# Kernel tuning notes

Hardware: AMD Instinct MI355X
Metric: run time of the kernel (lower is better)

Reference implementation:

```python
import jax, jax.numpy as jnp
import numpy as np

H = 16            # num_heads
SEG = 2048        # segment_size
DIL = 8           # dilation_rate
BLOCK_M = 64      # triton query block size (min(64, M_padded))


def setup_inputs() -> dict:
    key = jax.random.key(0)
    k1, k2, k3 = jax.random.split(key, 3)
    B, M, D = 2, 8192, 1024
    x = jax.random.normal(k1, (B, M, D), dtype=jnp.float32)
    Wqkv = jax.random.normal(k2, (3 * D, D), dtype=jnp.float32) * 0.02
    Wout = jax.random.normal(k3, (D, D), dtype=jnp.float32) * 0.02
    return {"x": x, "Wqkv": Wqkv, "Wout": Wout}


def reference(x, Wqkv, Wout):
    B, M, D = x.shape
    hd = D // H
    scale = hd ** -0.5
    S = M // SEG                      # number of segments (M is a multiple of SEG)
    Kn = SEG // DIL                   # dilated keys per segment
    nb = SEG // BLOCK_M               # query blocks per segment

    # qkv projection (torch Linear: x @ W^T), split into q,k,v: [B,H,M,hd]
    qkv = jnp.einsum('bmd,ed->bme', x, Wqkv).reshape(B, M, 3, H, hd)
    qkv = jnp.transpose(qkv, (2, 0, 3, 1, 4))
    q, k, v = qkv[0] * scale, qkv[1], qkv[2]

    # segment-local views
    q4 = q.reshape(B, H, S, SEG, hd)
    k4 = k.reshape(B, H, S, SEG, hd)[:, :, :, ::DIL]   # [B,H,S,Kn,hd] dilated keys
    v4 = v.reshape(B, H, S, SEG, hd)[:, :, :, ::DIL]

    # scores per segment: [B,H,S,SEG,Kn]
    scores = jnp.einsum('bhspd,bhskd->bhspk', q4, k4)
    # kernel normalization: per key j, subtract max over the 64-query block
    scores = scores.reshape(B, H, S, nb, BLOCK_M, Kn)
    c = jnp.max(scores, axis=4, keepdims=True)          # [B,H,S,nb,1,Kn]
    w = jnp.exp(scores - c)
    den = jnp.sum(w, axis=-1) + 1e-10                   # [B,H,S,nb,BLOCK_M]
    num = jnp.einsum('bhsnmk,bhskd->bhsnmd', w, v4)
    out = num / den[..., None]                          # [B,H,S,nb,BLOCK_M,hd]

    out = out.reshape(B, H, M, hd)
    out = jnp.transpose(out, (0, 2, 1, 3)).reshape(B, M, D)
    return jnp.einsum('bmd,ed->bme', out, Wout)
```

## Files before the change

### kernel.cpp

```cpp
#include <hip/hip_runtime.h>
#include <hip/hip_bf16.h>
#include <stdint.h>


typedef __attribute__((ext_vector_type(8))) short short8;
typedef __attribute__((ext_vector_type(4))) float f32x4;

#define DEVI static __device__ __forceinline__

DEVI unsigned short f2bf(float f) {
  union { float f; uint32_t u; } v; v.f = f;
  return (unsigned short)((v.u + 0x7FFFu + ((v.u >> 16) & 1u)) >> 16);
}

DEVI uint32_t pack_bf16(float lo, float hi) {
  return (uint32_t)f2bf(lo) | ((uint32_t)f2bf(hi) << 16);
}

DEVI uint32_t pack_hu(float lo, float hi) {
  union { float f; uint32_t u; } a, b; a.f = lo; b.f = hi;
  return ((a.u + 0x8000u) >> 16) | ((b.u + 0x8000u) & 0xFFFF0000u);
}

DEVI void gload_lds16(const void* g, void* l) {
  __builtin_amdgcn_global_load_lds((const __attribute__((address_space(1))) void*)g,
                                   (__attribute__((address_space(3))) void*)l,
                                   16, 0, 0);
}

__global__ void cvt_all(const float* __restrict__ x, const float* __restrict__ wqkv,
                        const float* __restrict__ wout,
                        unsigned short* __restrict__ xb, unsigned short* __restrict__ wqkvb,
                        unsigned short* __restrict__ woutb) {
  long i = ((long)blockIdx.x * 256 + threadIdx.x) * 4;
  const float* src; unsigned short* dst; long off;
  if (i < 16777216)          { src = x;    dst = xb;    off = i; }
  else if (i < 19922944)     { src = wqkv; dst = wqkvb; off = i - 16777216; }
  else                       { src = wout; dst = woutb; off = i - 19922944; }
  float4 f = *(const float4*)(src + off);
  uint2 o;
  o.x = (uint32_t)f2bf(f.x) | ((uint32_t)f2bf(f.y) << 16);
  o.y = (uint32_t)f2bf(f.z) | ((uint32_t)f2bf(f.w) << 16);
  *(uint2*)(dst + off) = o;
}

#define STAGE_A(bf, hf, kt) do { \
  gload_lds16(Abase + (long)((hf) * 128 + srow0) * 1024 + (kt) * 64 + scol0, &smA[bf][hf][se0]); \
  gload_lds16(Abase + (long)((hf) * 128 + srow1) * 1024 + (kt) * 64 + scol1, &smA[bf][hf][se1]); \
} while (0)
#define STAGE_B(bf, hf, kt) do { \
  gload_lds16(Bbase + (long)((hf) * 128 + srow0) * 1024 + (kt) * 64 + scol0, &smB[bf][hf][se0]); \
  gload_lds16(Bbase + (long)((hf) * 128 + srow1) * 1024 + (kt) * 64 + scol1, &smB[bf][hf][se1]); \
} while (0)

template<bool OUT_F32>
__global__ __launch_bounds__(512, 1) void gemm8p(
    const unsigned short* __restrict__ A, const unsigned short* __restrict__ B,
    void* __restrict__ Cv, float scale)
{
  __shared__ unsigned short smA[2][2][128 * 64];
  __shared__ unsigned short smB[2][2][128 * 64];
  const int tid = threadIdx.x;
  const int tm = blockIdx.x, tn = blockIdx.y;
  const int w = tid >> 6, lane = tid & 63;
  const int wm = w >> 2, wn = w & 3;
  const int lr = lane & 15, lq = lane >> 4;

  const int e0 = tid * 8,        e1 = (512 + tid) * 8;
  const int srow0 = e0 >> 6,     srow1 = e1 >> 6;
  const int sc0 = (e0 >> 3) & 7, sc1 = (e1 >> 3) & 7;
  const int scol0 = (sc0 ^ (srow0 & 7)) * 8, scol1 = (sc1 ^ (srow1 & 7)) * 8;
  const int se0 = e0, se1 = e1;

  const unsigned short* Abase = A + (long)tm * 256 * 1024;
  const unsigned short* Bbase = B + (long)tn * 256 * 1024;

  f32x4 acc[8][4] = {};
  short8 af[4][2];
  short8 bfr[2][2][2];

  STAGE_A(0, 0, 0); STAGE_B(0, 0, 0); STAGE_B(0, 1, 0); STAGE_A(0, 1, 0);
  asm volatile("s_waitcnt vmcnt(4)" ::: "memory");
  __builtin_amdgcn_s_barrier();
  asm volatile("" ::: "memory");

  for (int t = 0; t < 8; ++t) {
#pragma unroll
    for (int p = 0; p < 8; ++p) {
      const int o = p >> 2;
      const int q = p & 3;
      const int a = (p >> 1) & 1;
      const int b = a ^ (q & 1);

      if (q == 0 || q == 2) {
#pragma unroll
        for (int mi2 = 0; mi2 < 4; ++mi2) {
          int r = wm * 64 + mi2 * 16 + lr;
#pragma unroll
          for (int kk = 0; kk < 2; ++kk) {
            int kc = kk * 4 + lq;
            af[mi2][kk] = *(const short8*)&smA[o][a][r * 64 + ((kc ^ (r & 7)) * 8)];
          }
        }
      }
      if (q == 0 || q == 1) {
#pragma unroll
        for (int nj2 = 0; nj2 < 2; ++nj2) {
          int r = wn * 32 + nj2 * 16 + lr;
#pragma unroll
          for (int kk = 0; kk < 2; ++kk) {
            int kc = kk * 4 + lq;
            bfr[b][nj2][kk] = *(const short8*)&smB[o][b][r * 64 + ((kc ^ (r & 7)) * 8)];
          }
        }
      }

      switch (p) {
        case 0: STAGE_A(1, 0, 2 * t + 1); STAGE_B(1, 0, 2 * t + 1); break;
        case 2: STAGE_B(1, 1, 2 * t + 1); STAGE_A(1, 1, 2 * t + 1); break;
        case 4: if (t < 7) { STAGE_A(0, 0, 2 * t + 2); STAGE_B(0, 0, 2 * t + 2); } break;
        case 6: if (t < 7) { STAGE_B(0, 1, 2 * t + 2); STAGE_A(0, 1, 2 * t + 2); } break;
      }

      __builtin_amdgcn_s_barrier();
      asm volatile("" ::: "memory");

      __builtin_amdgcn_s_setprio(1);
#pragma unroll
      for (int kk = 0; kk < 2; ++kk)
#pragma unroll
        for (int mi2 = 0; mi2 < 4; ++mi2)
#pragma unroll
          for (int nj2 = 0; nj2 < 2; ++nj2)
            acc[a * 4 + mi2][b * 2 + nj2] = __builtin_amdgcn_mfma_f32_16x16x32_bf16(
                af[mi2][kk], bfr[b][nj2][kk], acc[a * 4 + mi2][b * 2 + nj2], 0, 0, 0);
      __builtin_amdgcn_s_setprio(0);

      if (t < 7) {
        if (p == 0 || p == 3 || p == 4 || p == 7)
          asm volatile("s_waitcnt vmcnt(4)" ::: "memory");
      } else {
        if (p == 0 || p == 3)  asm volatile("s_waitcnt vmcnt(4)" ::: "memory");
        else if (p == 4)       asm volatile("s_waitcnt vmcnt(0)" ::: "memory");
      }
      __builtin_amdgcn_s_barrier();
      asm volatile("" ::: "memory");
    }
  }

  if (OUT_F32) {
    float* scratch = (float*)&smA[0][0][0] + w * 544;
    float* Cf = (float*)Cv;
#pragma unroll
    for (int ai = 0; ai < 8; ++ai) {
#pragma unroll
      for (int b2 = 0; b2 < 2; ++b2) {
#pragma unroll
        for (int nj2 = 0; nj2 < 2; ++nj2)
#pragma unroll
          for (int rr = 0; rr < 4; ++rr)
            scratch[(lq * 4 + rr) * 33 + nj2 * 16 + lr] = acc[ai][b2 * 2 + nj2][rr] * scale;
        asm volatile("s_waitcnt lgkmcnt(0)" ::: "memory");
        __builtin_amdgcn_sched_barrier(0);
        int rr2 = lane >> 2, cb = (lane & 3) * 8;
        float4 v0, v1;
        v0.x = scratch[rr2 * 33 + cb + 0]; v0.y = scratch[rr2 * 33 + cb + 1];
        v0.z = scratch[rr2 * 33 + cb + 2]; v0.w = scratch[rr2 * 33 + cb + 3];
        v1.x = scratch[rr2 * 33 + cb + 4]; v1.y = scratch[rr2 * 33 + cb + 5];
        v1.z = scratch[rr2 * 33 + cb + 6]; v1.w = scratch[rr2 * 33 + cb + 7];
        asm volatile("s_waitcnt lgkmcnt(0)" ::: "memory");
        __builtin_amdgcn_sched_barrier(0);
        long rowg = tm * 256 + wm * 64 + (ai & 3) * 16 + (ai >> 2) * 128 + rr2;
        long colg = tn * 256 + wn * 32 + b2 * 128 + cb;
        *(float4*)&Cf[rowg * 1024 + colg] = v0;
        *(float4*)&Cf[rowg * 1024 + colg + 4] = v1;
      }
    }
  } else {
    const int row0 = tm * 256 + wm * 64 + lq * 4;
    const int col0 = tn * 256 + wn * 32 + lr;
#pragma unroll
    for (int mi = 0; mi < 8; ++mi) {
      int row = row0 + (mi & 3) * 16 + (mi >> 2) * 128;
#pragma unroll
      for (int nj = 0; nj < 4; ++nj) {
        int col = col0 + (nj & 1) * 16 + (nj >> 1) * 128;
#pragma unroll
        for (int rr = 0; rr < 4; ++rr)
          ((unsigned short*)Cv)[(long)(row + rr) * 1024 + col] = f2bf(acc[mi][nj][rr] * scale);
      }
    }
  }
}

template<int EPI>
__global__ __launch_bounds__(256, 2) void gemm_bt(
    const unsigned short* __restrict__ A, const unsigned short* __restrict__ B,
    void* __restrict__ Cv, unsigned short* __restrict__ Cv2,
    float scale, long a_row_stride, int ldc, int K)
{
  __shared__ unsigned short smA[128 * 64];
  __shared__ unsigned short smB[128 * 64];
  const int tid = threadIdx.x;
  const int tm = blockIdx.x, tn = blockIdx.y;
  const int w = tid >> 6, lane = tid & 63;
  const int wr = (w >> 1) * 64, wc = (w & 1) * 64;
  const int lr = lane & 15, lq = lane >> 4;

  int se[4], srow[4], scol[4];
#pragma unroll
  for (int i = 0; i < 4; ++i) {
    int e = (i * 256 + tid) * 8;
    int r = e >> 6;
    int cc = (e >> 3) & 7;
    se[i] = e; srow[i] = r; scol[i] = (cc ^ (r & 7)) * 8;
  }

  f32x4 acc[4][4] = {};

  for (int kt = 0; kt < K / 64; ++kt) {
    if (kt) __syncthreads();
#pragma unroll
    for (int i = 0; i < 4; ++i)
      gload_lds16(A + (long)(tm * 128 + srow[i]) * a_row_stride + kt * 64 + scol[i], &smA[se[i]]);
#pragma unroll
    for (int i = 0; i < 4; ++i)
      gload_lds16(B + (long)(tn * 128 + srow[i]) * K + kt * 64 + scol[i], &smB[se[i]]);
    __syncthreads();

#pragma unroll
    for (int kk = 0; kk < 2; ++kk) {
      int kc = kk * 4 + lq;
      short8 af[4], bfm[4];
#pragma unroll
      for (int i = 0; i < 4; ++i) {
        int row = wr + i * 16 + lr;
        af[i] = *(const short8*)&smA[row * 64 + ((kc ^ (row & 7)) * 8)];
      }
#pragma unroll
      for (int j = 0; j < 4; ++j) {
        int row = wc + j * 16 + lr;
        bfm[j] = *(const short8*)&smB[row * 64 + ((kc ^ (row & 7)) * 8)];
      }
#pragma unroll
      for (int i = 0; i < 4; ++i)
#pragma unroll
        for (int j = 0; j < 4; ++j)
          acc[i][j] = __builtin_amdgcn_mfma_f32_16x16x32_bf16(af[i], bfm[j], acc[i][j], 0, 0, 0);
    }
  }

  if (EPI == 2 && tn >= 8) {
    const int fbase = (tn - 8) * 128 + wc;
#pragma unroll
    for (int ip = 0; ip < 4; ip += 2) {
      int t0 = tm * 128 + wr + ip * 16 + lq * 4;
      int seg = t0 >> 8;
      int ts  = t0 & 255;
      int c32 = (ts >> 5) * 16 + (ts & 15);
#pragma unroll
      for (int j = 0; j < 4; ++j) {
        int f = fbase + j * 16 + lr;
        uint32_t* rp = (uint32_t*)&Cv2[((long)(seg * 1024 + f)) * 256];
        uint4 U;
        U.x = pack_bf16(acc[ip][j][0] * scale, acc[ip + 1][j][0] * scale);
        U.y = pack_bf16(acc[ip][j][1] * scale, acc[ip + 1][j][1] * scale);
        U.z = pack_bf16(acc[ip][j][2] * scale, acc[ip + 1][j][2] * scale);
        U.w = pack_bf16(acc[ip][j][3] * scale, acc[ip + 1][j][3] * scale);
        *(uint4*)&rp[c32] = U;
      }
    }
    return;
  }

#pragma unroll
  for (int i = 0; i < 4; ++i) {
    int rg0 = tm * 128 + wr + i * 16 + lq * 4;
#pragma unroll
    for (int j = 0; j < 4; ++j) {
      int cg = tn * 128 + wc + j * 16 + lr;
#pragma unroll
      for (int r = 0; r < 4; ++r) {
        float v = acc[i][j][r] * scale;
        long off = (long)(rg0 + r) * ldc + cg;
        if (EPI == 0) ((float*)Cv)[off] = v;
        else          ((unsigned short*)Cv)[off] = f2bf(v);
      }
    }
  }
}

__global__ __launch_bounds__(512, 2) void attn_kernel(
    const unsigned short* __restrict__ qb,
    const unsigned short* __restrict__ kb,
    const unsigned short* __restrict__ vtb,
    unsigned short* __restrict__ attout)
{
  __shared__ unsigned short v_t[64 * 256];
  __shared__ uint32_t w32[8][64][20];

  const int u = (blockIdx.x & 7) * 64 + (blockIdx.x >> 3);
  const int quarter = u & 3, h = (u >> 2) & 15, s = (u >> 6) & 3, b = u >> 8;
  const int tid = threadIdx.x, w = tid >> 6, lane = tid & 63;
  const int lr = lane & 15, lq = lane >> 4;
  const long qrow0 = (long)b * 8192 + s * 2048 + quarter * 512 + w * 64;
  const int hc = h * 64;

  const unsigned short* kbase = kb + ((long)(b * 4 + s) * 256) * 1024 + hc;
  const unsigned short* vbase = vtb + ((long)(b * 4 + s) * 1024 + hc) * 256;

#pragma unroll
  for (int it = 0; it < 4; ++it) {
    int e = (it * 512 + tid) * 8;
    int f = e >> 8;
    int ch = (e >> 3) & 31;
    gload_lds16(vbase + (long)f * 256 + ((ch ^ (f & 7)) * 8), &v_t[e]);
  }

  const unsigned short* qbase = qb + qrow0 * 1024 + hc;
  short8 aq[4][2];
#pragma unroll
  for (int i = 0; i < 4; ++i)
#pragma unroll
    for (int kk = 0; kk < 2; ++kk)
      aq[i][kk] = *(const short8*)&qbase[(i * 16 + lr) * 1024 + (kk * 4 + lq) * 8];

  __syncthreads();

  short8 ones;
#pragma unroll
  for (int e = 0; e < 8; ++e) ones[e] = (short)0x3F80;

  uint32_t (*wsl)[20] = w32[w];

  f32x4 acc_pv[4][4] = {};
  f32x4 acc_den[4] = {};
  short8 bk0[2][2], bk1[2][2];
  f32x4 sA[4][2], sB[4][2];

#define LOADK(BK, CC) do { \
  _Pragma("unroll") for (int j = 0; j < 2; ++j) \
    _Pragma("unroll") for (int kk = 0; kk < 2; ++kk) \
      BK[j][kk] = *(const short8*)&kbase[(long)((CC) * 32 + j * 16 + lr) * 1024 + (kk * 4 + lq) * 8]; \
} while (0)

#define QKT(S, BK) do { \
  _Pragma("unroll") for (int i = 0; i < 4; ++i) \
    _Pragma("unroll") for (int j = 0; j < 2; ++j) { \
      f32x4 z = {0.f, 0.f, 0.f, 0.f}; S[i][j] = z; } \
  _Pragma("unroll") for (int kk = 0; kk < 2; ++kk) \
    _Pragma("unroll") for (int i = 0; i < 4; ++i) \
      _Pragma("unroll") for (int j = 0; j < 2; ++j) \
        S[i][j] = __builtin_amdgcn_mfma_f32_16x16x32_bf16(aq[i][kk], BK[j][kk], S[i][j], 0, 0, 0); \
} while (0)

#define SOFTPV(S, CC) do { \
  short8 av_[4]; \
  _Pragma("unroll") for (int ct = 0; ct < 4; ++ct) { \
    int frow = ct * 16 + lr; \
    av_[ct] = *(const short8*)&v_t[frow * 256 + ((((CC) * 4 + lq) ^ (frow & 7)) << 3)]; } \
  float p0[4], p1[4]; \
  _Pragma("unroll") for (int i = 0; i < 4; ++i) { \
    p0[i] = fmaxf(fmaxf(S[i][0][0], S[i][0][1]), fmaxf(S[i][0][2], S[i][0][3])); \
    p1[i] = fmaxf(fmaxf(S[i][1][0], S[i][1][1]), fmaxf(S[i][1][2], S[i][1][3])); \
  } \
  float c0 = fmaxf(fmaxf(p0[0], p0[1]), fmaxf(p0[2], p0[3])); \
  float c1 = fmaxf(fmaxf(p1[0], p1[1]), fmaxf(p1[2], p1[3])); \
  c0 = fmaxf(c0, __shfl_xor(c0, 16)); c0 = fmaxf(c0, __shfl_xor(c0, 32)); \
  c1 = fmaxf(c1, __shfl_xor(c1, 16)); c1 = fmaxf(c1, __shfl_xor(c1, 32)); \
  _Pragma("unroll") for (int uu = 0; uu < 4; ++uu) { \
    _Pragma("unroll") for (int r = 0; r < 4; ++r) { \
      int qq = uu * 16 + lq * 4 + r; \
      wsl[qq][lr] = pack_hu(__expf(S[uu][0][r] - c0), __expf(S[uu][1][r] - c1)); } \
    short8 bw = *(const short8*)&wsl[uu * 16 + lr][lq * 4]; \
    acc_den[uu] = __builtin_amdgcn_mfma_f32_16x16x32_bf16(ones, bw, acc_den[uu], 0, 0, 0); \
    _Pragma("unroll") for (int ct = 0; ct < 4; ++ct) \
      acc_pv[uu][ct] = __builtin_amdgcn_mfma_f32_16x16x32_bf16(av_[ct], bw, acc_pv[uu][ct], 0, 0, 0); \
  } \
} while (0)

  LOADK(bk0, 0);
  LOADK(bk1, 1);
  QKT(sA, bk0);

  LOADK(bk0, 2); QKT(sB, bk1); SOFTPV(sA, 0);
  LOADK(bk1, 3); QKT(sA, bk0); SOFTPV(sB, 1);
  LOADK(bk0, 4); QKT(sB, bk1); SOFTPV(sA, 2);
  LOADK(bk1, 5); QKT(sA, bk0); SOFTPV(sB, 3);
  LOADK(bk0, 6); QKT(sB, bk1); SOFTPV(sA, 4);
  LOADK(bk1, 7); QKT(sA, bk0); SOFTPV(sB, 5);
                 QKT(sB, bk1); SOFTPV(sA, 6);
                               SOFTPV(sB, 7);

#pragma unroll
  for (int qi = 0; qi < 4; ++qi) {
    float inv = 1.0f / (acc_den[qi][0] + 1e-10f);
    long orow = (qrow0 + qi * 16 + lr) * 1024 + hc;
#pragma unroll
    for (int ct = 0; ct < 4; ++ct) {
      uint2 p;
      p.x = pack_hu(acc_pv[qi][ct][0] * inv, acc_pv[qi][ct][1] * inv);
      p.y = pack_hu(acc_pv[qi][ct][2] * inv, acc_pv[qi][ct][3] * inv);
      *(uint2*)&attout[orow + ct * 16 + lq * 4] = p;
    }
  }
}

extern "C" void kernel_launch(void* const* d_in, const int* in_sizes, int n_in,
                              void* d_out, int out_size, void* d_ws, size_t ws_size,
                              hipStream_t stream) {
  (void)in_sizes; (void)n_in; (void)out_size; (void)ws_size;
  const float* x    = (const float*)d_in[0];
  const float* Wqkv = (const float*)d_in[1];
  const float* Wout = (const float*)d_in[2];
  float* out = (float*)d_out;
  char* ws = (char*)d_ws;

  unsigned short* xb     = (unsigned short*)(ws);
  unsigned short* attout = (unsigned short*)(ws);
  unsigned short* wqkvb  = (unsigned short*)(ws + 33554432);
  unsigned short* woutb  = (unsigned short*)(ws + 39845888);
  unsigned short* qbuf   = (unsigned short*)(ws + 41943040);
  unsigned short* kbuf   = (unsigned short*)(ws + 75497472);
  unsigned short* vtb    = (unsigned short*)(ws + 79691776);

  cvt_all<<<20480, 256, 0, stream>>>(x, Wqkv, Wout, xb, wqkvb, woutb);

  gemm8p<false><<<dim3(64, 4), 512, 0, stream>>>(xb, wqkvb, (void*)qbuf, 0.125f);
  gemm_bt<2><<<dim3(16, 16), 256, 0, stream>>>(
      xb, wqkvb + 1024 * 1024, (void*)kbuf, vtb, 1.0f, 8192, 1024, 1024);

  attn_kernel<<<512, 512, 0, stream>>>(qbuf, kbuf, vtb, attout);

  gemm8p<true><<<dim3(64, 4), 512, 0, stream>>>(attout, woutb, (void*)out, 1.0f);
}
```

Measured before the change: 162.8 us.

## Merge Q and K/V projections into one launch; shrink attention blocks

The Q projection and the dilated K/V projection now run in a single 320-block launch. Blocks 0-255 compute Q with the 256x256 pipelined tile, and blocks 256-319 compute K and transposed V over only the dilated rows, reusing the same main loop (now shared through a macro). This removes one kernel launch and the weaker 128x128 gemm_bt path. The attention kernel is also split into 1024 blocks of 256 threads with occupancy hint 3, instead of 512 blocks of 512 threads, to improve load balance and occupancy. The trade-off is that the K/V blocks run a heavier tile serially alongside the Q blocks, and the attention kernel reloads the V tile twice as often.

```diff
diff --git a/kernel.cpp b/kernel.cpp
--- a/kernel.cpp
+++ b/kernel.cpp
@@ -44,24 +44,95 @@
   *(uint2*)(dst + off) = o;
 }
 
+#define GEMM8P_MAINLOOP(ASTRIDE)                                               \
+  f32x4 acc[8][4] = {};                                                        \
+  short8 af[4][2];                                                             \
+  short8 bfr[2][2][2];                                                         \
+  STAGE_A(0, 0, 0); STAGE_B(0, 0, 0); STAGE_B(0, 1, 0); STAGE_A(0, 1, 0);      \
+  asm volatile("s_waitcnt vmcnt(4)" ::: "memory");                             \
+  __builtin_amdgcn_s_barrier();                                                \
+  asm volatile("" ::: "memory");                                               \
+  for (int t = 0; t < 8; ++t) {                                                \
+    _Pragma("unroll")                                                          \
+    for (int p = 0; p < 8; ++p) {                                              \
+      const int o = p >> 2;                                                    \
+      const int q = p & 3;                                                     \
+      const int a = (p >> 1) & 1;                                              \
+      const int b = a ^ (q & 1);                                               \
+      if (q == 0 || q == 2) {                                                  \
+        _Pragma("unroll")                                                      \
+        for (int mi2 = 0; mi2 < 4; ++mi2) {                                    \
+          int r = wm * 64 + mi2 * 16 + lr;                                     \
+          _Pragma("unroll")                                                    \
+          for (int kk = 0; kk < 2; ++kk) {                                     \
+            int kc = kk * 4 + lq;                                              \
+            af[mi2][kk] = *(const short8*)&smA[o][a][r * 64 + ((kc ^ (r & 7)) * 8)]; \
+          }                                                                    \
+        }                                                                      \
+      }                                                                        \
+      if (q == 0 || q == 1) {                                                  \
+        _Pragma("unroll")                                                      \
+        for (int nj2 = 0; nj2 < 2; ++nj2) {                                    \
+          int r = wn * 32 + nj2 * 16 + lr;                                     \
+          _Pragma("unroll")                                                    \
+          for (int kk = 0; kk < 2; ++kk) {                                     \
+            int kc = kk * 4 + lq;                                              \
+            bfr[b][nj2][kk] = *(const short8*)&smB[o][b][r * 64 + ((kc ^ (r & 7)) * 8)]; \
+          }                                                                    \
+        }                                                                      \
+      }                                                                        \
+      switch (p) {                                                             \
+        case 0: STAGE_A(1, 0, 2 * t + 1); STAGE_B(1, 0, 2 * t + 1); break;     \
+        case 2: STAGE_B(1, 1, 2 * t + 1); STAGE_A(1, 1, 2 * t + 1); break;     \
+        case 4: if (t < 7) { STAGE_A(0, 0, 2 * t + 2); STAGE_B(0, 0, 2 * t + 2); } break; \
+        case 6: if (t < 7) { STAGE_B(0, 1, 2 * t + 2); STAGE_A(0, 1, 2 * t + 2); } break; \
+      }                                                                        \
+      __builtin_amdgcn_s_barrier();                                            \
+      asm volatile("" ::: "memory");                                           \
+      __builtin_amdgcn_s_setprio(1);                                           \
+      _Pragma("unroll")                                                        \
+      for (int kk = 0; kk < 2; ++kk)                                           \
+        _Pragma("unroll")                                                      \
+        for (int mi2 = 0; mi2 < 4; ++mi2)                                      \
+          _Pragma("unroll")                                                    \
+          for (int nj2 = 0; nj2 < 2; ++nj2)                                    \
+            acc[a * 4 + mi2][b * 2 + nj2] = __builtin_amdgcn_mfma_f32_16x16x32_bf16( \
+                af[mi2][kk], bfr[b][nj2][kk], acc[a * 4 + mi2][b * 2 + nj2], 0, 0, 0); \
+      __builtin_amdgcn_s_setprio(0);                                           \
+      if (t < 7) {                                                             \
+        if (p == 0 || p == 3 || p == 4 || p == 7)                              \
+          asm volatile("s_waitcnt vmcnt(4)" ::: "memory");                     \
+      } else {                                                                 \
+        if (p == 0 || p == 3)  asm volatile("s_waitcnt vmcnt(4)" ::: "memory"); \
+        else if (p == 4)       asm volatile("s_waitcnt vmcnt(0)" ::: "memory"); \
+      }                                                                        \
+      __builtin_amdgcn_s_barrier();                                            \
+      asm volatile("" ::: "memory");                                           \
+    }                                                                          \
+  }
+
 #define STAGE_A(bf, hf, kt) do { \
-  gload_lds16(Abase + (long)((hf) * 128 + srow0) * 1024 + (kt) * 64 + scol0, &smA[bf][hf][se0]); \
-  gload_lds16(Abase + (long)((hf) * 128 + srow1) * 1024 + (kt) * 64 + scol1, &smA[bf][hf][se1]); \
+  gload_lds16(Abase + (long)((hf) * 128 + srow0) * AST + (kt) * 64 + scol0, &smA[bf][hf][se0]); \
+  gload_lds16(Abase + (long)((hf) * 128 + srow1) * AST + (kt) * 64 + scol1, &smA[bf][hf][se1]); \
 } while (0)
 #define STAGE_B(bf, hf, kt) do { \
   gload_lds16(Bbase + (long)((hf) * 128 + srow0) * 1024 + (kt) * 64 + scol0, &smB[bf][hf][se0]); \
   gload_lds16(Bbase + (long)((hf) * 128 + srow1) * 1024 + (kt) * 64 + scol1, &smB[bf][hf][se1]); \
 } while (0)
 
-template<bool OUT_F32>
-__global__ __launch_bounds__(512, 1) void gemm8p(
-    const unsigned short* __restrict__ A, const unsigned short* __restrict__ B,
-    void* __restrict__ Cv, float scale)
+__global__ __launch_bounds__(512, 1) void gemm_qkv(
+    const unsigned short* __restrict__ xb, const unsigned short* __restrict__ wqkvb,
+    unsigned short* __restrict__ qbuf, unsigned short* __restrict__ kbuf,
+    unsigned short* __restrict__ vtb)
 {
   __shared__ unsigned short smA[2][2][128 * 64];
   __shared__ unsigned short smB[2][2][128 * 64];
+  const int bid = blockIdx.x;
+  const bool isQ = bid < 256;
+  const int tm = isQ ? (bid & 63) : ((bid - 256) & 7);
+  const int tn = isQ ? (bid >> 6) : ((bid - 256) >> 3);
+  const long AST = isQ ? 1024 : 8192;
   const int tid = threadIdx.x;
-  const int tm = blockIdx.x, tn = blockIdx.y;
   const int w = tid >> 6, lane = tid & 63;
   const int wm = w >> 2, wn = w & 3;
   const int lr = lane & 15, lq = lane >> 4;
@@ -72,111 +143,12 @@
   const int scol0 = (sc0 ^ (srow0 & 7)) * 8, scol1 = (sc1 ^ (srow1 & 7)) * 8;
   const int se0 = e0, se1 = e1;
 
-  const unsigned short* Abase = A + (long)tm * 256 * 1024;
-  const unsigned short* Bbase = B + (long)tn * 256 * 1024;
-
-  f32x4 acc[8][4] = {};
-  short8 af[4][2];
-  short8 bfr[2][2][2];
-
-  STAGE_A(0, 0, 0); STAGE_B(0, 0, 0); STAGE_B(0, 1, 0); STAGE_A(0, 1, 0);
-  asm volatile("s_waitcnt vmcnt(4)" ::: "memory");
-  __builtin_amdgcn_s_barrier();
-  asm volatile("" ::: "memory");
-
-  for (int t = 0; t < 8; ++t) {
-#pragma unroll
-    for (int p = 0; p < 8; ++p) {
-      const int o = p >> 2;
-      const int q = p & 3;
-      const int a = (p >> 1) & 1;
-      const int b = a ^ (q & 1);
-
-      if (q == 0 || q == 2) {
-#pragma unroll
-        for (int mi2 = 0; mi2 < 4; ++mi2) {
-          int r = wm * 64 + mi2 * 16 + lr;
-#pragma unroll
-          for (int kk = 0; kk < 2; ++kk) {
-            int kc = kk * 4 + lq;
-            af[mi2][kk] = *(const short8*)&smA[o][a][r * 64 + ((kc ^ (r & 7)) * 8)];
-          }
-        }
-      }
-      if (q == 0 || q == 1) {
-#pragma unroll
-        for (int nj2 = 0; nj2 < 2; ++nj2) {
-          int r = wn * 32 + nj2 * 16 + lr;
-#pragma unroll
-          for (int kk = 0; kk < 2; ++kk) {
-            int kc = kk * 4 + lq;
-            bfr[b][nj2][kk] = *(const short8*)&smB[o][b][r * 64 + ((kc ^ (r & 7)) * 8)];
-          }
-        }
-      }
-
-      switch (p) {
-        case 0: STAGE_A(1, 0, 2 * t + 1); STAGE_B(1, 0, 2 * t + 1); break;
-        case 2: STAGE_B(1, 1, 2 * t + 1); STAGE_A(1, 1, 2 * t + 1); break;
-        case 4: if (t < 7) { STAGE_A(0, 0, 2 * t + 2); STAGE_B(0, 0, 2 * t + 2); } break;
-        case 6: if (t < 7) { STAGE_B(0, 1, 2 * t + 2); STAGE_A(0, 1, 2 * t + 2); } break;
-      }
-
-      __builtin_amdgcn_s_barrier();
-      asm volatile("" ::: "memory");
-
-      __builtin_amdgcn_s_setprio(1);
-#pragma unroll
-      for (int kk = 0; kk < 2; ++kk)
-#pragma unroll
-        for (int mi2 = 0; mi2 < 4; ++mi2)
-#pragma unroll
-          for (int nj2 = 0; nj2 < 2; ++nj2)
-            acc[a * 4 + mi2][b * 2 + nj2] = __builtin_amdgcn_mfma_f32_16x16x32_bf16(
-                af[mi2][kk], bfr[b][nj2][kk], acc[a * 4 + mi2][b * 2 + nj2], 0, 0, 0);
-      __builtin_amdgcn_s_setprio(0);
-
-      if (t < 7) {
-        if (p == 0 || p == 3 || p == 4 || p == 7)
-          asm volatile("s_waitcnt vmcnt(4)" ::: "memory");
-      } else {
-        if (p == 0 || p == 3)  asm volatile("s_waitcnt vmcnt(4)" ::: "memory");
-        else if (p == 4)       asm volatile("s_waitcnt vmcnt(0)" ::: "memory");
-      }
-      __builtin_amdgcn_s_barrier();
-      asm volatile("" ::: "memory");
-    }
-  }
-
-  if (OUT_F32) {
-    float* scratch = (float*)&smA[0][0][0] + w * 544;
-    float* Cf = (float*)Cv;
-#pragma unroll
-    for (int ai = 0; ai < 8; ++ai) {
-#pragma unroll
-      for (int b2 = 0; b2 < 2; ++b2) {
-#pragma unroll
-        for (int nj2 = 0; nj2 < 2; ++nj2)
-#pragma unroll
-          for (int rr = 0; rr < 4; ++rr)
-            scratch[(lq * 4 + rr) * 33 + nj2 * 16 + lr] = acc[ai][b2 * 2 + nj2][rr] * scale;
-        asm volatile("s_waitcnt lgkmcnt(0)" ::: "memory");
-        __builtin_amdgcn_sched_barrier(0);
-        int rr2 = lane >> 2, cb = (lane & 3) * 8;
-        float4 v0, v1;
-        v0.x = scratch[rr2 * 33 + cb + 0]; v0.y = scratch[rr2 * 33 + cb + 1];
-        v0.z = scratch[rr2 * 33 + cb + 2]; v0.w = scratch[rr2 * 33 + cb + 3];
-        v1.x = scratch[rr2 * 33 + cb + 4]; v1.y = scratch[rr2 * 33 + cb + 5];
-        v1.z = scratch[rr2 * 33 + cb + 6]; v1.w = scratch[rr2 * 33 + cb + 7];
-        asm volatile("s_waitcnt lgkmcnt(0)" ::: "memory");
-        __builtin_amdgcn_sched_barrier(0);
-        long rowg = tm * 256 + wm * 64 + (ai & 3) * 16 + (ai >> 2) * 128 + rr2;
-        long colg = tn * 256 + wn * 32 + b2 * 128 + cb;
-        *(float4*)&Cf[rowg * 1024 + colg] = v0;
-        *(float4*)&Cf[rowg * 1024 + colg + 4] = v1;
-      }
-    }
-  } else {
+  const unsigned short* Abase = xb + (long)tm * 256 * AST;
+  const unsigned short* Bbase = (isQ ? wqkvb : wqkvb + 1024 * 1024) + (long)tn * 256 * 1024;
+
+  GEMM8P_MAINLOOP(AST)
+
+  if (isQ) {
     const int row0 = tm * 256 + wm * 64 + lq * 4;
     const int col0 = tn * 256 + wn * 32 + lr;
 #pragma unroll
@@ -187,131 +159,119 @@
         int col = col0 + (nj & 1) * 16 + (nj >> 1) * 128;
 #pragma unroll
         for (int rr = 0; rr < 4; ++rr)
-          ((unsigned short*)Cv)[(long)(row + rr) * 1024 + col] = f2bf(acc[mi][nj][rr] * scale);
+          qbuf[(long)(row + rr) * 1024 + col] = f2bf(acc[mi][nj][rr] * 0.125f);
       }
     }
-  }
-}
-
-template<int EPI>
-__global__ __launch_bounds__(256, 2) void gemm_bt(
-    const unsigned short* __restrict__ A, const unsigned short* __restrict__ B,
-    void* __restrict__ Cv, unsigned short* __restrict__ Cv2,
-    float scale, long a_row_stride, int ldc, int K)
-{
-  __shared__ unsigned short smA[128 * 64];
-  __shared__ unsigned short smB[128 * 64];
-  const int tid = threadIdx.x;
-  const int tm = blockIdx.x, tn = blockIdx.y;
-  const int w = tid >> 6, lane = tid & 63;
-  const int wr = (w >> 1) * 64, wc = (w & 1) * 64;
-  const int lr = lane & 15, lq = lane >> 4;
-
-  int se[4], srow[4], scol[4];
-#pragma unroll
-  for (int i = 0; i < 4; ++i) {
-    int e = (i * 256 + tid) * 8;
-    int r = e >> 6;
-    int cc = (e >> 3) & 7;
-    se[i] = e; srow[i] = r; scol[i] = (cc ^ (r & 7)) * 8;
-  }
-
-  f32x4 acc[4][4] = {};
-
-  for (int kt = 0; kt < K / 64; ++kt) {
-    if (kt) __syncthreads();
-#pragma unroll
-    for (int i = 0; i < 4; ++i)
-      gload_lds16(A + (long)(tm * 128 + srow[i]) * a_row_stride + kt * 64 + scol[i], &smA[se[i]]);
-#pragma unroll
-    for (int i = 0; i < 4; ++i)
-      gload_lds16(B + (long)(tn * 128 + srow[i]) * K + kt * 64 + scol[i], &smB[se[i]]);
-    __syncthreads();
-
-#pragma unroll
-    for (int kk = 0; kk < 2; ++kk) {
-      int kc = kk * 4 + lq;
-      short8 af[4], bfm[4];
-#pragma unroll
-      for (int i = 0; i < 4; ++i) {
-        int row = wr + i * 16 + lr;
-        af[i] = *(const short8*)&smA[row * 64 + ((kc ^ (row & 7)) * 8)];
+  } else if (tn < 4) {
+    const int row0 = tm * 256 + wm * 64 + lq * 4;
+    const int col0 = tn * 256 + wn * 32 + lr;
+#pragma unroll
+    for (int mi = 0; mi < 8; ++mi) {
+      int row = row0 + (mi & 3) * 16 + (mi >> 2) * 128;
+#pragma unroll
+      for (int nj = 0; nj < 4; ++nj) {
+        int col = col0 + (nj & 1) * 16 + (nj >> 1) * 128;
+#pragma unroll
+        for (int rr = 0; rr < 4; ++rr)
+          kbuf[(long)(row + rr) * 1024 + col] = f2bf(acc[mi][nj][rr]);
       }
-#pragma unroll
-      for (int j = 0; j < 4; ++j) {
-        int row = wc + j * 16 + lr;
-        bfm[j] = *(const short8*)&smB[row * 64 + ((kc ^ (row & 7)) * 8)];
-      }
-#pragma unroll
-      for (int i = 0; i < 4; ++i)
-#pragma unroll
-        for (int j = 0; j < 4; ++j)
-          acc[i][j] = __builtin_amdgcn_mfma_f32_16x16x32_bf16(af[i], bfm[j], acc[i][j], 0, 0, 0);
-    }
-  }
-
-  if (EPI == 2 && tn >= 8) {
-    const int fbase = (tn - 8) * 128 + wc;
-#pragma unroll
-    for (int ip = 0; ip < 4; ip += 2) {
-      int t0 = tm * 128 + wr + ip * 16 + lq * 4;
+    }
+  } else {
+#pragma unroll
+    for (int mi = 0; mi < 8; mi += 2) {
+      int t0 = tm * 256 + wm * 64 + (mi & 3) * 16 + (mi >> 2) * 128 + lq * 4;
       int seg = t0 >> 8;
       int ts  = t0 & 255;
       int c32 = (ts >> 5) * 16 + (ts & 15);
 #pragma unroll
-      for (int j = 0; j < 4; ++j) {
-        int f = fbase + j * 16 + lr;
-        uint32_t* rp = (uint32_t*)&Cv2[((long)(seg * 1024 + f)) * 256];
+      for (int nj = 0; nj < 4; ++nj) {
+        int f = (tn - 4) * 256 + wn * 32 + (nj & 1) * 16 + (nj >> 1) * 128 + lr;
+        uint32_t* rp = (uint32_t*)&vtb[((long)(seg * 1024 + f)) * 256];
         uint4 U;
-        U.x = pack_bf16(acc[ip][j][0] * scale, acc[ip + 1][j][0] * scale);
-        U.y = pack_bf16(acc[ip][j][1] * scale, acc[ip + 1][j][1] * scale);
-        U.z = pack_bf16(acc[ip][j][2] * scale, acc[ip + 1][j][2] * scale);
-        U.w = pack_bf16(acc[ip][j][3] * scale, acc[ip + 1][j][3] * scale);
+        U.x = pack_bf16(acc[mi][nj][0], acc[mi + 1][nj][0]);
+        U.y = pack_bf16(acc[mi][nj][1], acc[mi + 1][nj][1]);
+        U.z = pack_bf16(acc[mi][nj][2], acc[mi + 1][nj][2]);
+        U.w = pack_bf16(acc[mi][nj][3], acc[mi + 1][nj][3]);
         *(uint4*)&rp[c32] = U;
       }
     }
-    return;
-  }
-
-#pragma unroll
-  for (int i = 0; i < 4; ++i) {
-    int rg0 = tm * 128 + wr + i * 16 + lq * 4;
-#pragma unroll
-    for (int j = 0; j < 4; ++j) {
-      int cg = tn * 128 + wc + j * 16 + lr;
-#pragma unroll
-      for (int r = 0; r < 4; ++r) {
-        float v = acc[i][j][r] * scale;
-        long off = (long)(rg0 + r) * ldc + cg;
-        if (EPI == 0) ((float*)Cv)[off] = v;
-        else          ((unsigned short*)Cv)[off] = f2bf(v);
-      }
-    }
-  }
-}
-
-__global__ __launch_bounds__(512, 2) void attn_kernel(
+  }
+}
+
+__global__ __launch_bounds__(512, 1) void gemm_out(
+    const unsigned short* __restrict__ A, const unsigned short* __restrict__ B,
+    float* __restrict__ Cf)
+{
+  __shared__ unsigned short smA[2][2][128 * 64];
+  __shared__ unsigned short smB[2][2][128 * 64];
+  const int tm = blockIdx.x, tn = blockIdx.y;
+  const long AST = 1024;
+  const int tid = threadIdx.x;
+  const int w = tid >> 6, lane = tid & 63;
+  const int wm = w >> 2, wn = w & 3;
+  const int lr = lane & 15, lq = lane >> 4;
+
+  const int e0 = tid * 8,        e1 = (512 + tid) * 8;
+  const int srow0 = e0 >> 6,     srow1 = e1 >> 6;
+  const int sc0 = (e0 >> 3) & 7, sc1 = (e1 >> 3) & 7;
+  const int scol0 = (sc0 ^ (srow0 & 7)) * 8, scol1 = (sc1 ^ (srow1 & 7)) * 8;
+  const int se0 = e0, se1 = e1;
+
+  const unsigned short* Abase = A + (long)tm * 256 * 1024;
+  const unsigned short* Bbase = B + (long)tn * 256 * 1024;
+
+  GEMM8P_MAINLOOP(AST)
+
+  float* scratch = (float*)&smA[0][0][0] + w * 544;
+#pragma unroll
+  for (int ai = 0; ai < 8; ++ai) {
+#pragma unroll
+    for (int b2 = 0; b2 < 2; ++b2) {
+#pragma unroll
+      for (int nj2 = 0; nj2 < 2; ++nj2)
+#pragma unroll
+        for (int rr = 0; rr < 4; ++rr)
+          scratch[(lq * 4 + rr) * 33 + nj2 * 16 + lr] = acc[ai][b2 * 2 + nj2][rr];
+      asm volatile("s_waitcnt lgkmcnt(0)" ::: "memory");
+      __builtin_amdgcn_sched_barrier(0);
+      int rr2 = lane >> 2, cb = (lane & 3) * 8;
+      float4 v0, v1;
+      v0.x = scratch[rr2 * 33 + cb + 0]; v0.y = scratch[rr2 * 33 + cb + 1];
+      v0.z = scratch[rr2 * 33 + cb + 2]; v0.w = scratch[rr2 * 33 + cb + 3];
+      v1.x = scratch[rr2 * 33 + cb + 4]; v1.y = scratch[rr2 * 33 + cb + 5];
+      v1.z = scratch[rr2 * 33 + cb + 6]; v1.w = scratch[rr2 * 33 + cb + 7];
+      asm volatile("s_waitcnt lgkmcnt(0)" ::: "memory");
+      __builtin_amdgcn_sched_barrier(0);
+      long rowg = tm * 256 + wm * 64 + (ai & 3) * 16 + (ai >> 2) * 128 + rr2;
+      long colg = tn * 256 + wn * 32 + b2 * 128 + cb;
+      *(float4*)&Cf[rowg * 1024 + colg] = v0;
+      *(float4*)&Cf[rowg * 1024 + colg + 4] = v1;
+    }
+  }
+}
+
+__global__ __launch_bounds__(256, 3) void attn_kernel(
     const unsigned short* __restrict__ qb,
     const unsigned short* __restrict__ kb,
     const unsigned short* __restrict__ vtb,
     unsigned short* __restrict__ attout)
 {
   __shared__ unsigned short v_t[64 * 256];
-  __shared__ uint32_t w32[8][64][20];
-
-  const int u = (blockIdx.x & 7) * 64 + (blockIdx.x >> 3);
-  const int quarter = u & 3, h = (u >> 2) & 15, s = (u >> 6) & 3, b = u >> 8;
+  __shared__ uint32_t w32[4][64][20];
+
+  const int u = (blockIdx.x & 7) * 128 + (blockIdx.x >> 3);
+  const int e8 = u & 7, h = (u >> 3) & 15, s = (u >> 7) & 3, b = u >> 9;
   const int tid = threadIdx.x, w = tid >> 6, lane = tid & 63;
   const int lr = lane & 15, lq = lane >> 4;
-  const long qrow0 = (long)b * 8192 + s * 2048 + quarter * 512 + w * 64;
+  const long qrow0 = (long)b * 8192 + s * 2048 + e8 * 256 + w * 64;
   const int hc = h * 64;
 
   const unsigned short* kbase = kb + ((long)(b * 4 + s) * 256) * 1024 + hc;
   const unsigned short* vbase = vtb + ((long)(b * 4 + s) * 1024 + hc) * 256;
 
 #pragma unroll
-  for (int it = 0; it < 4; ++it) {
-    int e = (it * 512 + tid) * 8;
+  for (int it = 0; it < 8; ++it) {
+    int e = (it * 256 + tid) * 8;
     int f = e >> 8;
     int ch = (e >> 3) & 31;
     gload_lds16(vbase + (long)f * 256 + ((ch ^ (f & 7)) * 8), &v_t[e]);
@@ -426,11 +386,9 @@
 
   cvt_all<<<20480, 256, 0, stream>>>(x, Wqkv, Wout, xb, wqkvb, woutb);
 
-  gemm8p<false><<<dim3(64, 4), 512, 0, stream>>>(xb, wqkvb, (void*)qbuf, 0.125f);
-  gemm_bt<2><<<dim3(16, 16), 256, 0, stream>>>(
-      xb, wqkvb + 1024 * 1024, (void*)kbuf, vtb, 1.0f, 8192, 1024, 1024);
-
-  attn_kernel<<<512, 512, 0, stream>>>(qbuf, kbuf, vtb, attout);
-
-  gemm8p<true><<<dim3(64, 4), 512, 0, stream>>>(attout, woutb, (void*)out, 1.0f);
-}
+  gemm_qkv<<<320, 512, 0, stream>>>(xb, wqkvb, qbuf, kbuf, vtb);
+
+  attn_kernel<<<1024, 256, 0, stream>>>(qbuf, kbuf, vtb, attout);
+
+  gemm_out<<<dim3(64, 4), 512, 0, stream>>>(attout, woutb, out);
+}
```

Result: slower. 343.2 us (+110.7%).
